# Performance work log

Hardware: AMD Instinct MI355X
Metric: run time of the kernel (lower is better)

## Reference

```python
import jax, jax.numpy as jnp
import numpy as np

N, DEG, F, H, OUT = 50000, 16, 128, 128, 64


def _lstm_aggr(neigh, w_ih, w_hh, b_ih, b_hh):
    # neigh: [N, D, F] fixed-degree neighbor features; run LSTM over D steps,
    # return final hidden state [N, H] (PyG SAGEConv 'lstm' aggregation).
    n, d, f = neigh.shape
    h_dim = w_hh.shape[1]

    def step(carry, xt):
        h, c = carry
        gates = xt @ w_ih.T + b_ih + h @ w_hh.T + b_hh  # [N, 4H]
        i, fg, g, o = jnp.split(gates, 4, axis=-1)      # torch gate order i,f,g,o
        i = jax.nn.sigmoid(i)
        fg = jax.nn.sigmoid(fg)
        g = jnp.tanh(g)
        o = jax.nn.sigmoid(o)
        c = fg * c + i * g
        h = o * jnp.tanh(c)
        return (h, c), None

    h0 = jnp.zeros((n, h_dim), neigh.dtype)
    (h, _), _ = jax.lax.scan(step, (h0, h0), jnp.swapaxes(neigh, 0, 1))
    return h


def _sage_lstm(x, src, w_ih, w_hh, b_ih, b_hh, wl, bl, wr):
    # SAGEConv: out = lin_l(lstm_aggr(x[neighbors])) + lin_r(x)
    neigh = x[src]                                   # [N, D, F] gather
    aggr = _lstm_aggr(neigh, w_ih, w_hh, b_ih, b_hh)  # [N, H]
    return aggr @ wl.T + bl + x @ wr.T


def setup_inputs() -> dict:
    key = jax.random.key(0)
    ks = jax.random.split(key, 16)
    x = jax.random.normal(ks[0], (N, F), dtype=jnp.float32)
    # fixed-degree graph: dst = arange(N) each repeated DEG times (sorted, as
    # PyG lstm aggregation requires), src random -> edge_index [2, N*DEG]
    src = jax.random.randint(ks[1], (N * DEG,), 0, N, dtype=jnp.int64)
    dst = jnp.repeat(jnp.arange(N, dtype=jnp.int64), DEG)
    edge_index = jnp.stack([src, dst])
    s = 1.0 / np.sqrt(H)
    def u(k, shape):
        return jax.random.uniform(k, shape, jnp.float32, -s, s)
    params = {
        # layer 1 (input F -> hidden H)
        "w_ih1": u(ks[2], (4 * H, F)), "w_hh1": u(ks[3], (4 * H, H)),
        "b_ih1": u(ks[4], (4 * H,)), "b_hh1": u(ks[5], (4 * H,)),
        "lin_l1_w": u(ks[6], (H, H)), "lin_l1_b": u(ks[6], (H,)),
        "lin_r1_w": u(ks[7], (H, F)),
        # layer 2 (H -> H)
        "w_ih2": u(ks[8], (4 * H, H)), "w_hh2": u(ks[9], (4 * H, H)),
        "b_ih2": u(ks[10], (4 * H,)), "b_hh2": u(ks[11], (4 * H,)),
        "lin_l2_w": u(ks[12], (H, H)), "lin_l2_b": u(ks[12], (H,)),
        "lin_r2_w": u(ks[13], (H, H)),
        # output head
        "lin_w": u(ks[14], (OUT, H)), "lin_b": u(ks[15], (OUT,)),
    }
    return {"x": x, "edge_index": edge_index, **params}


def reference(x, edge_index,
              w_ih1, w_hh1, b_ih1, b_hh1, lin_l1_w, lin_l1_b, lin_r1_w,
              w_ih2, w_hh2, b_ih2, b_hh2, lin_l2_w, lin_l2_b, lin_r2_w,
              lin_w, lin_b):
    n = x.shape[0]
    deg = edge_index.shape[1] // n
    src = edge_index[0].reshape(n, deg)  # fixed-degree neighbor matrix
    h = _sage_lstm(x, src, w_ih1, w_hh1, b_ih1, b_hh1, lin_l1_w, lin_l1_b, lin_r1_w)
    h = jax.nn.relu(h)
    h = _sage_lstm(h, src, w_ih2, w_hh2, b_ih2, b_hh2, lin_l2_w, lin_l2_b, lin_r2_w)
    h = jax.nn.relu(h)
    return h @ lin_w.T + lin_b
```

## Files before the change

kernel.cpp:

```cpp
#include <hip/hip_runtime.h>
#include <stdint.h>

#define NN 50000
#define DEG 16
#define MT 16
#define NBLK ((NN + MT - 1) / MT)
#define LOG2E 1.4426950408889634f

typedef short bf16x8 __attribute__((ext_vector_type(8)));
typedef float f32x4 __attribute__((ext_vector_type(4)));
typedef unsigned short u16;
typedef unsigned int u32;

static __device__ __forceinline__ u16 f2bf(float f) {
  union { float f; u32 u; } v; v.f = f;
  u32 u = v.u + 0x7FFFu + ((v.u >> 16) & 1u);
  return (u16)(u >> 16);
}
static __device__ __forceinline__ float rcp_(float x) {
  return __builtin_amdgcn_rcpf(x);
}
static __device__ __forceinline__ float ex2_(float x) {
  return __builtin_amdgcn_exp2f(x);
}

__global__ void k_prep(const float* __restrict__ x, u16* __restrict__ xb,
                       const float* __restrict__ wih1, const float* __restrict__ whh1, u16* __restrict__ wpk1,
                       const float* __restrict__ wih2, const float* __restrict__ whh2, u16* __restrict__ wpk2,
                       const float* __restrict__ lr1, const float* __restrict__ ll1, u16* __restrict__ epk1,
                       const float* __restrict__ lr2, const float* __restrict__ ll2, u16* __restrict__ epk2,
                       const float* __restrict__ linw, u16* __restrict__ hpk,
                       const float* __restrict__ bi1, const float* __restrict__ bh1, float* __restrict__ bs1,
                       const float* __restrict__ bi2, const float* __restrict__ bh2, float* __restrict__ bs2) {
  int b = blockIdx.x;
  if (b < 128) {
    const float* wih = (b < 64) ? wih1 : wih2;
    const float* whh = (b < 64) ? whh1 : whh2;
    u16* wpk = (b < 64) ? wpk1 : wpk2;
    int t = (b & 63) * 256 + threadIdx.x;
    int lane = t & 63, kt = (t >> 6) & 7, g = (t >> 9) & 3, w = (t >> 11) & 7;
    int col = g * 128 + w * 16 + (lane & 15);
    int k0 = kt * 32 + (lane >> 4) * 8;
    float sc = (g == 2) ? 2.f * LOG2E : LOG2E;
#pragma unroll
    for (int j = 0; j < 8; ++j) {
      int k = k0 + j;
      float v = (k < 128) ? wih[col * 128 + k] : whh[col * 128 + k - 128];
      wpk[t * 8 + j] = f2bf(sc * v);
    }
  } else if (b < 160) {
    const float* lrw = (b < 144) ? lr1 : lr2;
    const float* llw = (b < 144) ? ll1 : ll2;
    u16* epk = (b < 144) ? epk1 : epk2;
    int t = ((b - 128) & 15) * 256 + threadIdx.x;
    int lane = t & 63, kt = (t >> 6) & 7, w = (t >> 9) & 7;
    int col = w * 16 + (lane & 15);
    int k0 = kt * 32 + (lane >> 4) * 8;
#pragma unroll
    for (int j = 0; j < 8; ++j) {
      int k = k0 + j;
      epk[t * 8 + j] = f2bf(k < 128 ? lrw[col * 128 + k] : llw[col * 128 + k - 128]);
    }
  } else if (b < 164) {
    int t = (b - 160) * 256 + threadIdx.x;
    int lane = t & 63, kt = (t >> 6) & 3, w = (t >> 8) & 3;
    int col = w * 16 + (lane & 15);
    int k0 = kt * 32 + (lane >> 4) * 8;
#pragma unroll
    for (int j = 0; j < 8; ++j) hpk[t * 8 + j] = f2bf(linw[col * 128 + k0 + j]);
  } else if (b < 168) {
    int t = (b - 164) * 256 + threadIdx.x;
    if (t < 1024) {
      int i = t & 511;
      float sc = ((i >> 7) == 2) ? 2.f * LOG2E : LOG2E;
      if (t < 512) bs1[i] = sc * (bi1[i] + bh1[i]);
      else bs2[i] = sc * (bi2[i] + bh2[i]);
    }
  } else {
    int i = (b - 168) * 256 + threadIdx.x;
    int stride = (gridDim.x - 168) * 256;
    for (; i < NN * 128 / 4; i += stride) {
      float4 v = ((const float4*)x)[i];
      ushort4 o;
      o.x = f2bf(v.x); o.y = f2bf(v.y); o.z = f2bf(v.z); o.w = f2bf(v.w);
      ((ushort4*)xb)[i] = o;
    }
  }
}


#define XLOAD(DCODE)                                                          \
  do {                                                                        \
    int idx_ = ((DCODE) < DEG) ? IDXT[(DCODE) * 16 + lr] : node0 + lr;        \
    const u16* b_ = xin + (size_t)idx_ * 128 + lh * 8;                        \
    xf[0] = *(const bf16x8*)(b_);                                             \
    xf[1] = *(const bf16x8*)(b_ + 32);                                        \
    xf[2] = *(const bf16x8*)(b_ + 64);                                        \
    xf[3] = *(const bf16x8*)(b_ + 96);                                        \
  } while (0)

#define XPART()                                                               \
  do {                                                                        \
    __builtin_amdgcn_s_setprio(1);                                            \
    _Pragma("unroll") for (int g = 0; g < 4; ++g)                             \
        acc[g] = (f32x4){gb[g], gb[g], gb[g], gb[g]};                         \
    _Pragma("unroll") for (int kt = 0; kt < 4; ++kt)                          \
        _Pragma("unroll") for (int g = 0; g < 4; ++g)                         \
            acc[g] = __builtin_amdgcn_mfma_f32_16x16x32_bf16(xf[kt], wreg[g][kt], acc[g], 0, 0, 0); \
    __builtin_amdgcn_s_setprio(0);                                            \
  } while (0)

#define EBAR()                                                                \
  do {                                                                        \
    asm volatile("s_waitcnt lgkmcnt(0)" ::: "memory");                        \
    __builtin_amdgcn_s_barrier();                                             \
    __builtin_amdgcn_sched_barrier(0);                                        \
  } while (0)

template <int L2>
__global__ __launch_bounds__(512, 2) void k_layer(
    const u16* __restrict__ xin, const int* __restrict__ src,
    const u16* __restrict__ wpk, const float* __restrict__ bsum,
    const u16* __restrict__ epk, const float* __restrict__ linlb,
    u16* __restrict__ hout, const u16* __restrict__ hpk,
    const float* __restrict__ linb, float* __restrict__ dout) {
  __shared__ __align__(16) u16 AH[2][MT * 128];
  __shared__ int IDXT[DEG * MT];

  const int tid = threadIdx.x;
  const int w = tid >> 6, l = tid & 63;
  const int lr = l & 15, lh = l >> 4;
  const int node0 = blockIdx.x * MT;

  bf16x8 wreg[4][8];
#pragma unroll
  for (int g = 0; g < 4; ++g)
#pragma unroll
    for (int kt = 0; kt < 8; ++kt)
      wreg[g][kt] = *(const bf16x8*)(wpk + (size_t)(((w * 4 + g) * 8 + kt) * 64 + l) * 8);

  if (tid < MT * DEG) {
    IDXT[(tid & 15) * 16 + (tid >> 4)] = src[node0 * DEG + tid];
  }

  float gb[4];
#pragma unroll
  for (int g = 0; g < 4; ++g) gb[g] = bsum[g * 128 + w * 16 + lr];
  float eb = linlb[w * 16 + lr];
  __syncthreads();

  bf16x8 xf[4];
  f32x4 acc[4];
  f32x4 c4 = (f32x4){0.f, 0.f, 0.f, 0.f};

  XLOAD(0);
  XPART();
  XLOAD(1);

#pragma unroll 1
  for (int step = 0; step < DEG; ++step) {
    const int cb = step & 1, nb = cb ^ 1;

    if (step) {
      __builtin_amdgcn_s_setprio(1);
#pragma unroll
      for (int kt = 0; kt < 4; ++kt) {
        bf16x8 af = *(const bf16x8*)((const char*)AH[cb] + lr * 256 +
                                     ((kt * 64 + lh * 16) ^ ((lr & 15) << 4)));
#pragma unroll
        for (int g = 0; g < 4; ++g)
          acc[g] = __builtin_amdgcn_mfma_f32_16x16x32_bf16(af, wreg[g][4 + kt], acc[g], 0, 0, 0);
      }
      __builtin_amdgcn_s_setprio(0);
    }

#pragma unroll
    for (int r = 0; r < 4; ++r) {
      float iv = rcp_(1.f + ex2_(-acc[0][r]));
      float fv = rcp_(1.f + ex2_(-acc[1][r]));
      float gv = 1.f - 2.f * rcp_(1.f + ex2_(acc[2][r]));
      float ov = rcp_(1.f + ex2_(-acc[3][r]));
      float cv = fv * c4[r] + iv * gv;
      c4[r] = cv;
      float th = 1.f - 2.f * rcp_(1.f + ex2_(2.f * LOG2E * cv));
      int row = lh * 4 + r;
      int jj = 2 * (w * 16 + lr);
      *(u16*)((char*)AH[nb] + row * 256 + (jj ^ ((row & 15) << 4))) =
          f2bf(ov * th);
    }

    if (step < DEG - 1) {
      XPART();
      XLOAD(step + 2);
    }

    EBAR();
  }

  f32x4 eacc = (f32x4){eb, eb, eb, eb};
#pragma unroll
  for (int kt = 0; kt < 4; ++kt) {
    bf16x8 bf = *(const bf16x8*)(epk + (size_t)((w * 8 + kt) * 64 + l) * 8);
    eacc = __builtin_amdgcn_mfma_f32_16x16x32_bf16(xf[kt], bf, eacc, 0, 0, 0);
  }
#pragma unroll
  for (int kt = 0; kt < 4; ++kt) {
    bf16x8 af = *(const bf16x8*)((const char*)AH[0] + lr * 256 +
                                 ((kt * 64 + lh * 16) ^ ((lr & 15) << 4)));
    bf16x8 bf = *(const bf16x8*)(epk + (size_t)((w * 8 + 4 + kt) * 64 + l) * 8);
    eacc = __builtin_amdgcn_mfma_f32_16x16x32_bf16(af, bf, eacc, 0, 0, 0);
  }

  if constexpr (!L2) {
#pragma unroll
    for (int r = 0; r < 4; ++r) {
      int node = node0 + lh * 4 + r;
      float v = fmaxf(eacc[r], 0.f);
      hout[(size_t)node * 128 + w * 16 + lr] = f2bf(v);
    }
  } else {
#pragma unroll
    for (int r = 0; r < 4; ++r) {
      int row = lh * 4 + r;
      float v = fmaxf(eacc[r], 0.f);
      int jj = 2 * (w * 16 + lr);
      *(u16*)((char*)AH[1] + row * 256 + (jj ^ ((row & 15) << 4))) = f2bf(v);
    }
    __syncthreads();
    if (w < 4) {
      float hb = linb[w * 16 + lr];
      f32x4 hacc = (f32x4){hb, hb, hb, hb};
#pragma unroll
      for (int kt = 0; kt < 4; ++kt) {
        bf16x8 af = *(const bf16x8*)((const char*)AH[1] + lr * 256 +
                                     ((kt * 64 + lh * 16) ^ ((lr & 15) << 4)));
        bf16x8 bf = *(const bf16x8*)(hpk + (size_t)((w * 4 + kt) * 64 + l) * 8);
        hacc = __builtin_amdgcn_mfma_f32_16x16x32_bf16(af, bf, hacc, 0, 0, 0);
      }
#pragma unroll
      for (int r = 0; r < 4; ++r) {
        int node = node0 + lh * 4 + r;
        dout[(size_t)node * 64 + w * 16 + lr] = hacc[r];
      }
    }
  }
}

extern "C" void kernel_launch(void* const* d_in, const int* in_sizes, int n_in,
                              void* d_out, int out_size, void* d_ws, size_t ws_size,
                              hipStream_t stream) {
  const float* x    = (const float*)d_in[0];
  const int*   edge = (const int*)d_in[1];
  const float* wih1 = (const float*)d_in[2];
  const float* whh1 = (const float*)d_in[3];
  const float* bih1 = (const float*)d_in[4];
  const float* bhh1 = (const float*)d_in[5];
  const float* ll1w = (const float*)d_in[6];
  const float* ll1b = (const float*)d_in[7];
  const float* lr1w = (const float*)d_in[8];
  const float* wih2 = (const float*)d_in[9];
  const float* whh2 = (const float*)d_in[10];
  const float* bih2 = (const float*)d_in[11];
  const float* bhh2 = (const float*)d_in[12];
  const float* ll2w = (const float*)d_in[13];
  const float* ll2b = (const float*)d_in[14];
  const float* lr2w = (const float*)d_in[15];
  const float* linw = (const float*)d_in[16];
  const float* linb = (const float*)d_in[17];

  char* ws = (char*)d_ws;
  u16* xb    = (u16*)(ws);
  u16* h1b   = (u16*)(ws + 12800000);
  u16* wpk1  = (u16*)(ws + 25600000);
  u16* wpk2  = (u16*)(ws + 25862144);
  u16* epk1  = (u16*)(ws + 26124288);
  u16* epk2  = (u16*)(ws + 26189824);
  u16* hpk   = (u16*)(ws + 26255360);
  float* bs1 = (float*)(ws + 26271744);
  float* bs2 = (float*)(ws + 26273792);

  k_prep<<<1000, 256, 0, stream>>>(x, xb,
                                   wih1, whh1, wpk1, wih2, whh2, wpk2,
                                   lr1w, ll1w, epk1, lr2w, ll2w, epk2,
                                   linw, hpk,
                                   bih1, bhh1, bs1, bih2, bhh2, bs2);
  k_layer<0><<<NBLK, 512, 0, stream>>>(xb, edge, wpk1, bs1, epk1, ll1b,
                                       h1b, nullptr, nullptr, nullptr);
  k_layer<1><<<NBLK, 512, 0, stream>>>(h1b, edge, wpk2, bs2, epk2, ll2b,
                                       nullptr, hpk, linb, (float*)d_out);
}
```

Measured before the change: 563.1 us.

## Precompute input-gate projections per node once, then gather them in the LSTM

The x@W_ih projection is computed once per node (N rows) in a new k_gx kernel and stored as bf16, instead of once per edge (N*DEG rows) inside the recurrence. The layer kernel then gathers the precomputed gate rows into LDS with async global_load_lds over a triple buffer, and only does the h@W_hh MFMA per step. This halves the weight registers, which allows occupancy 4. The cost is an extra kernel launch, 51MB of workspace traffic per layer, and bf16 rounding of the gate pre-activations. There is a fallback path when the workspace is too small.

```diff
diff --git a/kernel.cpp b/kernel.cpp
--- a/kernel.cpp
+++ b/kernel.cpp
@@ -4,8 +4,11 @@
 #define NN 50000
 #define DEG 16
 #define MT 16
-#define NBLK ((NN + MT - 1) / MT)
+#define NBLK (NN / MT)
+#define MTG 64
+#define NBLKG ((NN + MTG - 1) / MTG)
 #define LOG2E 1.4426950408889634f
+#define GXR 520
 
 typedef short bf16x8 __attribute__((ext_vector_type(8)));
 typedef float f32x4 __attribute__((ext_vector_type(4)));
@@ -22,6 +25,14 @@
 }
 static __device__ __forceinline__ float ex2_(float x) {
   return __builtin_amdgcn_exp2f(x);
+}
+static __device__ __forceinline__ float bfhi2f(u32 hibits) {
+  union { u32 u; float f; } v; v.u = hibits; return v.f;
+}
+static __device__ __forceinline__ void gload_lds16(const void* g, void* l) {
+  __builtin_amdgcn_global_load_lds(
+      (const __attribute__((address_space(1))) void*)g,
+      (__attribute__((address_space(3))) void*)l, 16, 0, 0);
 }
 
 __global__ void k_prep(const float* __restrict__ x, u16* __restrict__ xb,
@@ -88,8 +99,217 @@
   }
 }
 
-
-#define XLOAD(DCODE)                                                          \
+__global__ __launch_bounds__(512, 2) void k_gx(
+    const u16* __restrict__ xin, const u16* __restrict__ wpk,
+    const float* __restrict__ bsum, u16* __restrict__ gx) {
+  const int tid = threadIdx.x;
+  const int w = tid >> 6, l = tid & 63;
+  const int lr = l & 15, lh = l >> 4;
+  const int node0 = blockIdx.x * MTG;
+
+  bf16x8 wreg[4][4];
+#pragma unroll
+  for (int g = 0; g < 4; ++g)
+#pragma unroll
+    for (int kt = 0; kt < 4; ++kt)
+      wreg[g][kt] = *(const bf16x8*)(wpk + (size_t)(((w * 4 + g) * 8 + kt) * 64 + l) * 8);
+
+  float gb[4];
+#pragma unroll
+  for (int g = 0; g < 4; ++g) gb[g] = bsum[g * 128 + w * 16 + lr];
+
+#pragma unroll
+  for (int mt = 0; mt < 4; ++mt) {
+    int anode = node0 + mt * 16 + lr;
+    if (anode >= NN) anode = NN - 1;
+    const u16* b_ = xin + (size_t)anode * 128 + lh * 8;
+    bf16x8 xf[4];
+#pragma unroll
+    for (int kt = 0; kt < 4; ++kt) xf[kt] = *(const bf16x8*)(b_ + kt * 32);
+    f32x4 acc[4];
+#pragma unroll
+    for (int g = 0; g < 4; ++g) acc[g] = (f32x4){gb[g], gb[g], gb[g], gb[g]};
+#pragma unroll
+    for (int kt = 0; kt < 4; ++kt)
+#pragma unroll
+      for (int g = 0; g < 4; ++g)
+        acc[g] = __builtin_amdgcn_mfma_f32_16x16x32_bf16(xf[kt], wreg[g][kt], acc[g], 0, 0, 0);
+#pragma unroll
+    for (int r = 0; r < 4; ++r) {
+      int nd = node0 + mt * 16 + lh * 4 + r;
+      if (nd < NN) {
+        u32 lo = (u32)f2bf(acc[0][r]) | ((u32)f2bf(acc[1][r]) << 16);
+        u32 hi = (u32)f2bf(acc[2][r]) | ((u32)f2bf(acc[3][r]) << 16);
+        *(uint2*)((char*)gx + (size_t)nd * 1024 + w * 128 + lr * 8) =
+            make_uint2(lo, hi);
+      }
+    }
+  }
+}
+
+
+#define STAGE(S, B)                                                           \
+  do {                                                                        \
+    _Pragma("unroll") for (int p = 0; p < 2; ++p) {                           \
+      int row_ = 2 * w + p;                                                   \
+      int idx_ = IDXT[(S) * 16 + row_];                                       \
+      gload_lds16((const char*)gxg + (size_t)idx_ * 1024 + l * 16,            \
+                  GXS[B] + row_ * GXR);                                       \
+    }                                                                         \
+  } while (0)
+
+#define CBAR(N)                                                               \
+  do {                                                                        \
+    asm volatile("s_waitcnt vmcnt(" #N ") lgkmcnt(0)" ::: "memory");          \
+    __builtin_amdgcn_s_barrier();                                             \
+    __builtin_amdgcn_sched_barrier(0);                                        \
+  } while (0)
+
+template <int L2>
+__global__ __launch_bounds__(512, 4) void k_layer_gx(
+    const u16* __restrict__ xin, const int* __restrict__ src,
+    const u16* __restrict__ wpk, const u16* __restrict__ gxg,
+    const u16* __restrict__ epk, const float* __restrict__ linlb,
+    u16* __restrict__ hout, const u16* __restrict__ hpk,
+    const float* __restrict__ linb, float* __restrict__ dout) {
+  __shared__ __align__(16) u16 GXS[3][MT * GXR];
+  __shared__ __align__(16) u16 AH[2][MT * 128];
+  __shared__ int IDXT[DEG * MT];
+
+  const int tid = threadIdx.x;
+  const int w = tid >> 6, l = tid & 63;
+  const int lr = l & 15, lh = l >> 4;
+  const int node0 = blockIdx.x * MT;
+
+  bf16x8 wreg[4][4];
+#pragma unroll
+  for (int g = 0; g < 4; ++g)
+#pragma unroll
+    for (int kt = 0; kt < 4; ++kt)
+      wreg[g][kt] = *(const bf16x8*)(wpk + (size_t)(((w * 4 + g) * 8 + 4 + kt) * 64 + l) * 8);
+
+  if (tid < MT * DEG)
+    IDXT[(tid & 15) * 16 + (tid >> 4)] = src[node0 * DEG + tid];
+
+  float eb = linlb[w * 16 + lr];
+  __syncthreads();
+
+  STAGE(0, 0);
+  STAGE(1, 1);
+
+  f32x4 acc[4];
+#pragma unroll
+  for (int g = 0; g < 4; ++g) acc[g] = (f32x4){0.f, 0.f, 0.f, 0.f};
+  f32x4 c4 = (f32x4){0.f, 0.f, 0.f, 0.f};
+  bf16x8 xf[4];
+
+  CBAR(2);
+
+#pragma unroll 1
+  for (int step = 0; step < DEG; ++step) {
+    const int cb = step & 1, nb = cb ^ 1;
+    const int sb = step % 3;
+
+    if (step < DEG - 2) {
+      const int b2 = (step + 2) % 3;
+      STAGE(step + 2, b2);
+    }
+    if (step == DEG - 1) {
+      const u16* b_ = xin + (size_t)(node0 + lr) * 128 + lh * 8;
+#pragma unroll
+      for (int kt = 0; kt < 4; ++kt) xf[kt] = *(const bf16x8*)(b_ + kt * 32);
+    }
+
+    if (step) {
+      __builtin_amdgcn_s_setprio(1);
+#pragma unroll
+      for (int kt = 0; kt < 4; ++kt) {
+        bf16x8 af = *(const bf16x8*)((const char*)AH[cb] + lr * 256 +
+                                     ((kt * 64 + lh * 16) ^ ((lr & 15) << 4)));
+#pragma unroll
+        for (int g = 0; g < 4; ++g)
+          acc[g] = __builtin_amdgcn_mfma_f32_16x16x32_bf16(af, wreg[g][kt], acc[g], 0, 0, 0);
+      }
+      __builtin_amdgcn_s_setprio(0);
+    }
+
+#pragma unroll
+    for (int r = 0; r < 4; ++r) {
+      int row = lh * 4 + r;
+      uint2 gv = *(const uint2*)((const char*)GXS[sb] + row * (GXR * 2) +
+                                 w * 128 + lr * 8);
+      float ai = acc[0][r] + bfhi2f(gv.x << 16);
+      float afv = acc[1][r] + bfhi2f(gv.x & 0xFFFF0000u);
+      float ag = acc[2][r] + bfhi2f(gv.y << 16);
+      float ao = acc[3][r] + bfhi2f(gv.y & 0xFFFF0000u);
+      float iv = rcp_(1.f + ex2_(-ai));
+      float fv = rcp_(1.f + ex2_(-afv));
+      float gvv = 1.f - 2.f * rcp_(1.f + ex2_(ag));
+      float ov = rcp_(1.f + ex2_(-ao));
+      float cv = fv * c4[r] + iv * gvv;
+      c4[r] = cv;
+      float th = 1.f - 2.f * rcp_(1.f + ex2_(2.f * LOG2E * cv));
+      int jj = 2 * (w * 16 + lr);
+      *(u16*)((char*)AH[nb] + row * 256 + (jj ^ ((row & 15) << 4))) =
+          f2bf(ov * th);
+    }
+#pragma unroll
+    for (int g = 0; g < 4; ++g) acc[g] = (f32x4){0.f, 0.f, 0.f, 0.f};
+
+    if (step < DEG - 2) CBAR(2);
+    else CBAR(0);
+  }
+
+  f32x4 eacc = (f32x4){eb, eb, eb, eb};
+#pragma unroll
+  for (int kt = 0; kt < 4; ++kt) {
+    bf16x8 bf = *(const bf16x8*)(epk + (size_t)((w * 8 + kt) * 64 + l) * 8);
+    eacc = __builtin_amdgcn_mfma_f32_16x16x32_bf16(xf[kt], bf, eacc, 0, 0, 0);
+  }
+#pragma unroll
+  for (int kt = 0; kt < 4; ++kt) {
+    bf16x8 af = *(const bf16x8*)((const char*)AH[0] + lr * 256 +
+                                 ((kt * 64 + lh * 16) ^ ((lr & 15) << 4)));
+    bf16x8 bf = *(const bf16x8*)(epk + (size_t)((w * 8 + 4 + kt) * 64 + l) * 8);
+    eacc = __builtin_amdgcn_mfma_f32_16x16x32_bf16(af, bf, eacc, 0, 0, 0);
+  }
+
+  if constexpr (!L2) {
+#pragma unroll
+    for (int r = 0; r < 4; ++r) {
+      int node = node0 + lh * 4 + r;
+      float v = fmaxf(eacc[r], 0.f);
+      hout[(size_t)node * 128 + w * 16 + lr] = f2bf(v);
+    }
+  } else {
+#pragma unroll
+    for (int r = 0; r < 4; ++r) {
+      int row = lh * 4 + r;
+      float v = fmaxf(eacc[r], 0.f);
+      int jj = 2 * (w * 16 + lr);
+      *(u16*)((char*)AH[1] + row * 256 + (jj ^ ((row & 15) << 4))) = f2bf(v);
+    }
+    __syncthreads();
+    if (w < 4) {
+      float hb = linb[w * 16 + lr];
+      f32x4 hacc = (f32x4){hb, hb, hb, hb};
+#pragma unroll
+      for (int kt = 0; kt < 4; ++kt) {
+        bf16x8 af = *(const bf16x8*)((const char*)AH[1] + lr * 256 +
+                                     ((kt * 64 + lh * 16) ^ ((lr & 15) << 4)));
+        bf16x8 bf = *(const bf16x8*)(hpk + (size_t)((w * 4 + kt) * 64 + l) * 8);
+        hacc = __builtin_amdgcn_mfma_f32_16x16x32_bf16(af, bf, hacc, 0, 0, 0);
+      }
+#pragma unroll
+      for (int r = 0; r < 4; ++r) {
+        int node = node0 + lh * 4 + r;
+        dout[(size_t)node * 64 + w * 16 + lr] = hacc[r];
+      }
+    }
+  }
+}
+
+#define FBXLOAD(DCODE)                                                        \
   do {                                                                        \
     int idx_ = ((DCODE) < DEG) ? IDXT[(DCODE) * 16 + lr] : node0 + lr;        \
     const u16* b_ = xin + (size_t)idx_ * 128 + lh * 8;                        \
@@ -99,7 +319,7 @@
     xf[3] = *(const bf16x8*)(b_ + 96);                                        \
   } while (0)
 
-#define XPART()                                                               \
+#define FBXPART()                                                             \
   do {                                                                        \
     __builtin_amdgcn_s_setprio(1);                                            \
     _Pragma("unroll") for (int g = 0; g < 4; ++g)                             \
@@ -110,7 +330,7 @@
     __builtin_amdgcn_s_setprio(0);                                            \
   } while (0)
 
-#define EBAR()                                                                \
+#define FBEBAR()                                                              \
   do {                                                                        \
     asm volatile("s_waitcnt lgkmcnt(0)" ::: "memory");                        \
     __builtin_amdgcn_s_barrier();                                             \
@@ -118,7 +338,7 @@
   } while (0)
 
 template <int L2>
-__global__ __launch_bounds__(512, 2) void k_layer(
+__global__ __launch_bounds__(512, 2) void k_layer_fb(
     const u16* __restrict__ xin, const int* __restrict__ src,
     const u16* __restrict__ wpk, const float* __restrict__ bsum,
     const u16* __restrict__ epk, const float* __restrict__ linlb,
@@ -139,9 +359,8 @@
     for (int kt = 0; kt < 8; ++kt)
       wreg[g][kt] = *(const bf16x8*)(wpk + (size_t)(((w * 4 + g) * 8 + kt) * 64 + l) * 8);
 
-  if (tid < MT * DEG) {
+  if (tid < MT * DEG)
     IDXT[(tid & 15) * 16 + (tid >> 4)] = src[node0 * DEG + tid];
-  }
 
   float gb[4];
 #pragma unroll
@@ -153,14 +372,13 @@
   f32x4 acc[4];
   f32x4 c4 = (f32x4){0.f, 0.f, 0.f, 0.f};
 
-  XLOAD(0);
-  XPART();
-  XLOAD(1);
+  FBXLOAD(0);
+  FBXPART();
+  FBXLOAD(1);
 
 #pragma unroll 1
   for (int step = 0; step < DEG; ++step) {
     const int cb = step & 1, nb = cb ^ 1;
-
     if (step) {
       __builtin_amdgcn_s_setprio(1);
 #pragma unroll
@@ -173,7 +391,6 @@
       }
       __builtin_amdgcn_s_setprio(0);
     }
-
 #pragma unroll
     for (int r = 0; r < 4; ++r) {
       float iv = rcp_(1.f + ex2_(-acc[0][r]));
@@ -188,13 +405,11 @@
       *(u16*)((char*)AH[nb] + row * 256 + (jj ^ ((row & 15) << 4))) =
           f2bf(ov * th);
     }
-
     if (step < DEG - 1) {
-      XPART();
-      XLOAD(step + 2);
-    }
-
-    EBAR();
+      FBXPART();
+      FBXLOAD(step + 2);
+    }
+    FBEBAR();
   }
 
   f32x4 eacc = (f32x4){eb, eb, eb, eb};
@@ -278,14 +493,25 @@
   u16* hpk   = (u16*)(ws + 26255360);
   float* bs1 = (float*)(ws + 26271744);
   float* bs2 = (float*)(ws + 26273792);
+  u16* gxb   = (u16*)(ws + 26280000);
+  const size_t need = 26280000ull + 51200000ull;
 
   k_prep<<<1000, 256, 0, stream>>>(x, xb,
                                    wih1, whh1, wpk1, wih2, whh2, wpk2,
                                    lr1w, ll1w, epk1, lr2w, ll2w, epk2,
                                    linw, hpk,
                                    bih1, bhh1, bs1, bih2, bhh2, bs2);
-  k_layer<0><<<NBLK, 512, 0, stream>>>(xb, edge, wpk1, bs1, epk1, ll1b,
-                                       h1b, nullptr, nullptr, nullptr);
-  k_layer<1><<<NBLK, 512, 0, stream>>>(h1b, edge, wpk2, bs2, epk2, ll2b,
-                                       nullptr, hpk, linb, (float*)d_out);
-}
+  if (ws_size >= need) {
+    k_gx<<<NBLKG, 512, 0, stream>>>(xb, wpk1, bs1, gxb);
+    k_layer_gx<0><<<NBLK, 512, 0, stream>>>(xb, edge, wpk1, gxb, epk1, ll1b,
+                                            h1b, nullptr, nullptr, nullptr);
+    k_gx<<<NBLKG, 512, 0, stream>>>(h1b, wpk2, bs2, gxb);
+    k_layer_gx<1><<<NBLK, 512, 0, stream>>>(h1b, edge, wpk2, gxb, epk2, ll2b,
+                                            nullptr, hpk, linb, (float*)d_out);
+  } else {
+    k_layer_fb<0><<<NBLK, 512, 0, stream>>>(xb, edge, wpk1, bs1, epk1, ll1b,
+                                            h1b, nullptr, nullptr, nullptr);
+    k_layer_fb<1><<<NBLK, 512, 0, stream>>>(h1b, edge, wpk2, bs2, epk2, ll2b,
+                                            nullptr, hpk, linb, (float*)d_out);
+  }
+}
```

Result: slower. 683.8 us (+21.5%).

## Process two 16-node tiles per block to interleave recurrent chains

Applied to the files above, without the earlier changes.

Each block now handles 32 nodes as two independent 16-row sub-tiles (A and B) that share the register-resident LSTM weights. The elementwise gate math of one sub-tile is interleaved with the MFMA input projection of the other, so the serial recurrence has independent work to hide latency behind. This halves the number of blocks and the per-node cost of loading weights into registers. In exchange it doubles accumulator and input registers per thread, which may cause spills or lower occupancy at launch_bounds(512,2), and it adds tail bounds checks for the partial last block.

```diff
diff --git a/kernel.cpp b/kernel.cpp
--- a/kernel.cpp
+++ b/kernel.cpp
@@ -3,7 +3,7 @@
 
 #define NN 50000
 #define DEG 16
-#define MT 16
+#define MT 32
 #define NBLK ((NN + MT - 1) / MT)
 #define LOG2E 1.4426950408889634f
 
@@ -89,25 +89,54 @@
 }
 
 
-#define XLOAD(DCODE)                                                          \
-  do {                                                                        \
-    int idx_ = ((DCODE) < DEG) ? IDXT[(DCODE) * 16 + lr] : node0 + lr;        \
+#define XLOADS(XF, DCODE, ROFF)                                               \
+  do {                                                                        \
+    int idx_;                                                                 \
+    if ((DCODE) < DEG) idx_ = IDXT[(DCODE) * 32 + (ROFF) + lr];               \
+    else { idx_ = node0 + (ROFF) + lr; if (idx_ >= NN) idx_ = NN - 1; }       \
     const u16* b_ = xin + (size_t)idx_ * 128 + lh * 8;                        \
-    xf[0] = *(const bf16x8*)(b_);                                             \
-    xf[1] = *(const bf16x8*)(b_ + 32);                                        \
-    xf[2] = *(const bf16x8*)(b_ + 64);                                        \
-    xf[3] = *(const bf16x8*)(b_ + 96);                                        \
-  } while (0)
-
-#define XPART()                                                               \
+    XF[0] = *(const bf16x8*)(b_);                                             \
+    XF[1] = *(const bf16x8*)(b_ + 32);                                        \
+    XF[2] = *(const bf16x8*)(b_ + 64);                                        \
+    XF[3] = *(const bf16x8*)(b_ + 96);                                        \
+  } while (0)
+
+#define XPARTS(ACC, XF)                                                       \
   do {                                                                        \
     __builtin_amdgcn_s_setprio(1);                                            \
     _Pragma("unroll") for (int g = 0; g < 4; ++g)                             \
-        acc[g] = (f32x4){gb[g], gb[g], gb[g], gb[g]};                         \
+        ACC[g] = (f32x4){gb[g], gb[g], gb[g], gb[g]};                         \
     _Pragma("unroll") for (int kt = 0; kt < 4; ++kt)                          \
         _Pragma("unroll") for (int g = 0; g < 4; ++g)                         \
-            acc[g] = __builtin_amdgcn_mfma_f32_16x16x32_bf16(xf[kt], wreg[g][kt], acc[g], 0, 0, 0); \
+            ACC[g] = __builtin_amdgcn_mfma_f32_16x16x32_bf16(XF[kt], wreg[g][kt], ACC[g], 0, 0, 0); \
     __builtin_amdgcn_s_setprio(0);                                            \
+  } while (0)
+
+#define HPARTS(ACC, AHSRC)                                                    \
+  do {                                                                        \
+    _Pragma("unroll") for (int kt = 0; kt < 4; ++kt) {                        \
+      bf16x8 af = *(const bf16x8*)((const char*)(AHSRC) + lr * 256 +          \
+                                   ((kt * 64 + lh * 16) ^ ((lr & 15) << 4))); \
+      _Pragma("unroll") for (int g = 0; g < 4; ++g)                           \
+        ACC[g] = __builtin_amdgcn_mfma_f32_16x16x32_bf16(af, wreg[g][4 + kt], ACC[g], 0, 0, 0); \
+    }                                                                         \
+  } while (0)
+
+#define EWS(ACC, C4, AHDST)                                                   \
+  do {                                                                        \
+    _Pragma("unroll") for (int r = 0; r < 4; ++r) {                           \
+      float iv = rcp_(1.f + ex2_(-ACC[0][r]));                                \
+      float fv = rcp_(1.f + ex2_(-ACC[1][r]));                                \
+      float gv = 1.f - 2.f * rcp_(1.f + ex2_(ACC[2][r]));                     \
+      float ov = rcp_(1.f + ex2_(-ACC[3][r]));                                \
+      float cv = fv * C4[r] + iv * gv;                                        \
+      C4[r] = cv;                                                             \
+      float th = 1.f - 2.f * rcp_(1.f + ex2_(2.f * LOG2E * cv));              \
+      int row = lh * 4 + r;                                                   \
+      int jj = 2 * (w * 16 + lr);                                             \
+      *(u16*)((char*)(AHDST) + row * 256 + (jj ^ ((row & 15) << 4))) =        \
+          f2bf(ov * th);                                                      \
+    }                                                                         \
   } while (0)
 
 #define EBAR()                                                                \
@@ -124,7 +153,8 @@
     const u16* __restrict__ epk, const float* __restrict__ linlb,
     u16* __restrict__ hout, const u16* __restrict__ hpk,
     const float* __restrict__ linb, float* __restrict__ dout) {
-  __shared__ __align__(16) u16 AH[2][MT * 128];
+  __shared__ __align__(16) u16 AHA[2][16 * 128];
+  __shared__ __align__(16) u16 AHB[2][16 * 128];
   __shared__ int IDXT[DEG * MT];
 
   const int tid = threadIdx.x;
@@ -139,8 +169,9 @@
     for (int kt = 0; kt < 8; ++kt)
       wreg[g][kt] = *(const bf16x8*)(wpk + (size_t)(((w * 4 + g) * 8 + kt) * 64 + l) * 8);
 
-  if (tid < MT * DEG) {
-    IDXT[(tid & 15) * 16 + (tid >> 4)] = src[node0 * DEG + tid];
+  {
+    int node = node0 + (tid >> 4);
+    IDXT[(tid & 15) * 32 + (tid >> 4)] = (node < NN) ? src[node * DEG + (tid & 15)] : 0;
   }
 
   float gb[4];
@@ -149,13 +180,17 @@
   float eb = linlb[w * 16 + lr];
   __syncthreads();
 
-  bf16x8 xf[4];
-  f32x4 acc[4];
-  f32x4 c4 = (f32x4){0.f, 0.f, 0.f, 0.f};
-
-  XLOAD(0);
-  XPART();
-  XLOAD(1);
+  bf16x8 xfA[4], xfB[4];
+  f32x4 accA[4], accB[4];
+  f32x4 cA = (f32x4){0.f, 0.f, 0.f, 0.f};
+  f32x4 cB = (f32x4){0.f, 0.f, 0.f, 0.f};
+
+  XLOADS(xfA, 0, 0);
+  XLOADS(xfB, 0, 16);
+  XPARTS(accA, xfA);
+  XPARTS(accB, xfB);
+  XLOADS(xfA, 1, 0);
+  XLOADS(xfB, 1, 16);
 
 #pragma unroll 1
   for (int step = 0; step < DEG; ++step) {
@@ -163,84 +198,82 @@
 
     if (step) {
       __builtin_amdgcn_s_setprio(1);
-#pragma unroll
-      for (int kt = 0; kt < 4; ++kt) {
-        bf16x8 af = *(const bf16x8*)((const char*)AH[cb] + lr * 256 +
-                                     ((kt * 64 + lh * 16) ^ ((lr & 15) << 4)));
-#pragma unroll
-        for (int g = 0; g < 4; ++g)
-          acc[g] = __builtin_amdgcn_mfma_f32_16x16x32_bf16(af, wreg[g][4 + kt], acc[g], 0, 0, 0);
-      }
+      HPARTS(accA, AHA[cb]);
+      HPARTS(accB, AHB[cb]);
       __builtin_amdgcn_s_setprio(0);
     }
 
+    EWS(accA, cA, AHA[nb]);
+    if (step < DEG - 1) {
+      XPARTS(accA, xfA);
+      XLOADS(xfA, step + 2, 0);
+    }
+    EWS(accB, cB, AHB[nb]);
+    if (step < DEG - 1) {
+      XPARTS(accB, xfB);
+      XLOADS(xfB, step + 2, 16);
+    }
+
+    EBAR();
+  }
+
+  f32x4 eaccA = (f32x4){eb, eb, eb, eb};
+  f32x4 eaccB = (f32x4){eb, eb, eb, eb};
+#pragma unroll
+  for (int kt = 0; kt < 4; ++kt) {
+    bf16x8 bf = *(const bf16x8*)(epk + (size_t)((w * 8 + kt) * 64 + l) * 8);
+    eaccA = __builtin_amdgcn_mfma_f32_16x16x32_bf16(xfA[kt], bf, eaccA, 0, 0, 0);
+    eaccB = __builtin_amdgcn_mfma_f32_16x16x32_bf16(xfB[kt], bf, eaccB, 0, 0, 0);
+  }
+#pragma unroll
+  for (int kt = 0; kt < 4; ++kt) {
+    int ofs = (kt * 64 + lh * 16) ^ ((lr & 15) << 4);
+    bf16x8 afA = *(const bf16x8*)((const char*)AHA[0] + lr * 256 + ofs);
+    bf16x8 afB = *(const bf16x8*)((const char*)AHB[0] + lr * 256 + ofs);
+    bf16x8 bf = *(const bf16x8*)(epk + (size_t)((w * 8 + 4 + kt) * 64 + l) * 8);
+    eaccA = __builtin_amdgcn_mfma_f32_16x16x32_bf16(afA, bf, eaccA, 0, 0, 0);
+    eaccB = __builtin_amdgcn_mfma_f32_16x16x32_bf16(afB, bf, eaccB, 0, 0, 0);
+  }
+
+  if constexpr (!L2) {
 #pragma unroll
     for (int r = 0; r < 4; ++r) {
-      float iv = rcp_(1.f + ex2_(-acc[0][r]));
-      float fv = rcp_(1.f + ex2_(-acc[1][r]));
-      float gv = 1.f - 2.f * rcp_(1.f + ex2_(acc[2][r]));
-      float ov = rcp_(1.f + ex2_(-acc[3][r]));
-      float cv = fv * c4[r] + iv * gv;
-      c4[r] = cv;
-      float th = 1.f - 2.f * rcp_(1.f + ex2_(2.f * LOG2E * cv));
+      int nodeA = node0 + lh * 4 + r;
+      int nodeB = node0 + 16 + lh * 4 + r;
+      if (nodeA < NN)
+        hout[(size_t)nodeA * 128 + w * 16 + lr] = f2bf(fmaxf(eaccA[r], 0.f));
+      if (nodeB < NN)
+        hout[(size_t)nodeB * 128 + w * 16 + lr] = f2bf(fmaxf(eaccB[r], 0.f));
+    }
+  } else {
+#pragma unroll
+    for (int r = 0; r < 4; ++r) {
       int row = lh * 4 + r;
       int jj = 2 * (w * 16 + lr);
-      *(u16*)((char*)AH[nb] + row * 256 + (jj ^ ((row & 15) << 4))) =
-          f2bf(ov * th);
-    }
-
-    if (step < DEG - 1) {
-      XPART();
-      XLOAD(step + 2);
-    }
-
-    EBAR();
-  }
-
-  f32x4 eacc = (f32x4){eb, eb, eb, eb};
-#pragma unroll
-  for (int kt = 0; kt < 4; ++kt) {
-    bf16x8 bf = *(const bf16x8*)(epk + (size_t)((w * 8 + kt) * 64 + l) * 8);
-    eacc = __builtin_amdgcn_mfma_f32_16x16x32_bf16(xf[kt], bf, eacc, 0, 0, 0);
-  }
-#pragma unroll
-  for (int kt = 0; kt < 4; ++kt) {
-    bf16x8 af = *(const bf16x8*)((const char*)AH[0] + lr * 256 +
-                                 ((kt * 64 + lh * 16) ^ ((lr & 15) << 4)));
-    bf16x8 bf = *(const bf16x8*)(epk + (size_t)((w * 8 + 4 + kt) * 64 + l) * 8);
-    eacc = __builtin_amdgcn_mfma_f32_16x16x32_bf16(af, bf, eacc, 0, 0, 0);
-  }
-
-  if constexpr (!L2) {
-#pragma unroll
-    for (int r = 0; r < 4; ++r) {
-      int node = node0 + lh * 4 + r;
-      float v = fmaxf(eacc[r], 0.f);
-      hout[(size_t)node * 128 + w * 16 + lr] = f2bf(v);
-    }
-  } else {
-#pragma unroll
-    for (int r = 0; r < 4; ++r) {
-      int row = lh * 4 + r;
-      float v = fmaxf(eacc[r], 0.f);
-      int jj = 2 * (w * 16 + lr);
-      *(u16*)((char*)AH[1] + row * 256 + (jj ^ ((row & 15) << 4))) = f2bf(v);
+      *(u16*)((char*)AHA[1] + row * 256 + (jj ^ ((row & 15) << 4))) =
+          f2bf(fmaxf(eaccA[r], 0.f));
+      *(u16*)((char*)AHB[1] + row * 256 + (jj ^ ((row & 15) << 4))) =
+          f2bf(fmaxf(eaccB[r], 0.f));
     }
     __syncthreads();
-    if (w < 4) {
-      float hb = linb[w * 16 + lr];
+    {
+      const u16* stash = (w < 4) ? AHB[1] : AHA[1];
+      stash = (w < 4) ? AHA[1] : AHB[1];
+      int w0 = w & 3;
+      int roff = (w < 4) ? 0 : 16;
+      float hb = linb[w0 * 16 + lr];
       f32x4 hacc = (f32x4){hb, hb, hb, hb};
 #pragma unroll
       for (int kt = 0; kt < 4; ++kt) {
-        bf16x8 af = *(const bf16x8*)((const char*)AH[1] + lr * 256 +
+        bf16x8 af = *(const bf16x8*)((const char*)stash + lr * 256 +
                                      ((kt * 64 + lh * 16) ^ ((lr & 15) << 4)));
-        bf16x8 bf = *(const bf16x8*)(hpk + (size_t)((w * 4 + kt) * 64 + l) * 8);
+        bf16x8 bf = *(const bf16x8*)(hpk + (size_t)((w0 * 4 + kt) * 64 + l) * 8);
         hacc = __builtin_amdgcn_mfma_f32_16x16x32_bf16(af, bf, hacc, 0, 0, 0);
       }
 #pragma unroll
       for (int r = 0; r < 4; ++r) {
-        int node = node0 + lh * 4 + r;
-        dout[(size_t)node * 64 + w * 16 + lr] = hacc[r];
+        int node = node0 + roff + lh * 4 + r;
+        if (node < NN) dout[(size_t)node * 64 + w0 * 16 + lr] = hacc[r];
       }
     }
   }
```

After: 648.7 us. 15.2% more time.
